# Performance work log

Hardware: AMD Instinct MI355X
Metric: run time of the kernel (lower is better)

## Reference

```python
import jax, jax.numpy as jnp
import numpy as np

E = 8        # num experts
TOPK = 2
H = 1024     # hidden size
F = 4096     # ffn hidden size
SL, BS = 2048, 2
TOKENS = SL * BS
N = TOKENS * TOPK          # flattened routing assignments
CAP = (TOPK * TOKENS) // E # expert_capacity with capacity_factor=1.0


def setup_inputs() -> dict:
    key = jax.random.key(0)
    ks = jax.random.split(key, 6)
    x = jax.random.normal(ks[0], (SL, BS, H), jnp.float32)
    scores = jax.random.uniform(ks[1], (TOKENS, E), dtype=jnp.float32)
    expert_weights = jax.random.uniform(ks[2], (TOKENS, TOPK), dtype=jnp.float32)
    top_experts = jax.random.randint(ks[3], (TOKENS, TOPK), 0, E, dtype=jnp.int32)
    w1 = jax.random.normal(ks[4], (E, H, F), jnp.float32) * 0.02
    w2 = jax.random.normal(ks[5], (E, F, H), jnp.float32) * 0.02
    bias = jnp.zeros((H,), jnp.float32)
    return {"x": x, "scores": scores, "expert_weights": expert_weights,
            "top_experts": top_experts, "w1": w1, "w2": w2, "bias": bias}


def reference(x, scores, expert_weights, top_experts, w1, w2, bias):
    # --- indices_and_bins: stable sort tokens by expert, histogram, cumsum ---
    te = top_experts.reshape(-1)          # [N] int
    ew = expert_weights.reshape(-1)       # [N]
    xf = x.reshape(-1, H)                 # [TOKENS, H]

    indices = jnp.argsort(te)             # stable sort -> permutation [N]
    bin_ids = te[indices]                 # sorted expert ids [N]
    tpe = jax.ops.segment_sum(jnp.ones_like(te), te, num_segments=E)  # tokens per expert
    bins = jnp.cumsum(tpe)                # inclusive cumsum
    starts = bins - tpe                   # start offset of each expert's bin
    pos = jnp.arange(N) - starts[bin_ids] # position within expert bin [N]
    valid = pos < CAP                     # capacity drop mask
    tok = indices // TOPK                 # source token row for each assignment

    # --- binned_gather: [E, CAP, H], zero padded, tokens beyond capacity dropped ---
    dst = jnp.where(valid, pos, CAP)      # out-of-range -> dropped via mode='drop'
    buf = jnp.zeros((E, CAP, H), x.dtype).at[bin_ids, dst].set(xf[tok], mode='drop')

    # --- grouped MLP: per-expert gelu FFN ---
    h = jax.nn.gelu(jnp.einsum('ech,ehf->ecf', buf, w1), approximate=False)
    y = jnp.einsum('ecf,efh->ech', h, w2)

    # --- binned_scatter: weighted un-permute back to token order ---
    vals = y[bin_ids, jnp.where(valid, pos, 0)]                      # [N, H]
    w = jnp.where(valid, ew[indices], 0.0)[:, None]
    out = jnp.zeros((TOKENS, H), x.dtype).at[tok].add(vals * w)

    return out.reshape(x.shape) + bias
```

## Files before the change

### kernel.cpp

```cpp
#include <hip/hip_runtime.h>
#include <hip/hip_bf16.h>
#include <math.h>

#define NE 8
#define TOPK 2
#define HD 1024
#define FD 4096
#define NTOK 4096
#define NASSIGN 8192
#define CAP 1024

typedef __attribute__((ext_vector_type(8))) short short8;
typedef __attribute__((ext_vector_type(4))) float f32x4;
typedef __attribute__((ext_vector_type(4))) unsigned short us4;
typedef __attribute__((ext_vector_type(4))) unsigned int u32x4;

__device__ __forceinline__ unsigned short f2bf(float f) {
  unsigned u = __float_as_uint(f);
  u += 0x7fffu + ((u >> 16) & 1u);
  return (unsigned short)(u >> 16);
}

__device__ __forceinline__ void load_lds16(const void* g, void* l) {
  __builtin_amdgcn_global_load_lds((const __attribute__((address_space(1))) void*)g,
                                   (__attribute__((address_space(3))) void*)l, 16, 0, 0);
}

__global__ __launch_bounds__(256)
void transpose_convert(const float* __restrict__ W, unsigned short* __restrict__ Wt,
                       int R, int C) {
  __shared__ float tile[64][65];
  int e = blockIdx.z;
  W  += (size_t)e * R * C;
  Wt += (size_t)e * R * C;
  int c0 = blockIdx.x * 64, r0 = blockIdx.y * 64;
  int tx = threadIdx.x & 15, ty = threadIdx.x >> 4;
#pragma unroll
  for (int i = 0; i < 4; ++i) {
    f32x4 v = *(const f32x4*)(W + (size_t)(r0 + ty + i * 16) * C + c0 + tx * 4);
    tile[ty + i * 16][tx * 4 + 0] = v.x;
    tile[ty + i * 16][tx * 4 + 1] = v.y;
    tile[ty + i * 16][tx * 4 + 2] = v.z;
    tile[ty + i * 16][tx * 4 + 3] = v.w;
  }
  __syncthreads();
#pragma unroll
  for (int i = 0; i < 4; ++i) {
    int c = ty + i * 16;
    us4 o;
    o.x = f2bf(tile[tx * 4 + 0][c]);
    o.y = f2bf(tile[tx * 4 + 1][c]);
    o.z = f2bf(tile[tx * 4 + 2][c]);
    o.w = f2bf(tile[tx * 4 + 3][c]);
    *(us4*)(Wt + (size_t)(c0 + c) * R + r0 + tx * 4) = o;
  }
}

__global__ __launch_bounds__(1024)
void routing_kernel(const int* __restrict__ te, int* __restrict__ rankA,
                    int* __restrict__ srcTok, int* __restrict__ counts) {
  __shared__ uint4 pref[1024];
  int t = threadIdx.x;
  int myTe[8];
  unsigned lc[4] = {0, 0, 0, 0};
#pragma unroll
  for (int j = 0; j < 8; ++j) {
    int ee = te[t * 8 + j];
    myTe[j] = ee;
    lc[ee >> 1] += 1u << ((ee & 1) * 16);
  }
  uint4 inc;
  inc.x = lc[0]; inc.y = lc[1]; inc.z = lc[2]; inc.w = lc[3];
  pref[t] = inc;
  __syncthreads();
  for (int d = 1; d < 1024; d <<= 1) {
    uint4 add;
    bool has = (t >= d);
    if (has) add = pref[t - d];
    __syncthreads();
    if (has) {
      inc.x += add.x; inc.y += add.y; inc.z += add.z; inc.w += add.w;
      pref[t] = inc;
    }
    __syncthreads();
  }
  unsigned ex[4] = {inc.x - lc[0], inc.y - lc[1], inc.z - lc[2], inc.w - lc[3]};
  uint4 tot = pref[1023];
  int run[8];
#pragma unroll
  for (int eidx = 0; eidx < 8; ++eidx)
    run[eidx] = (ex[eidx >> 1] >> ((eidx & 1) * 16)) & 0xffff;
#pragma unroll
  for (int j = 0; j < 8; ++j) {
    int ee = myTe[j];
    int r = run[ee]++;
    rankA[t * 8 + j] = r;
    if (r < CAP) srcTok[ee * CAP + r] = (t * 8 + j) >> 1;
  }
  if (t < 8) {
    unsigned tt[4] = {tot.x, tot.y, tot.z, tot.w};
    counts[t] = (tt[t >> 1] >> ((t & 1) * 16)) & 0xffff;
  }
}

__global__ __launch_bounds__(128)
void gather_kernel(const float* __restrict__ x, const int* __restrict__ srcTok,
                   const int* __restrict__ counts, unsigned short* __restrict__ buf) {
  int row = blockIdx.x;
  int e = row >> 10;
  int c = row & (CAP - 1);
  int t = threadIdx.x;
  unsigned short* dst = buf + (size_t)row * HD + t * 8;
  if (c < counts[e]) {
    const float* src = x + (size_t)srcTok[row] * HD + t * 8;
    f32x4 v0 = *(const f32x4*)src;
    f32x4 v1 = *(const f32x4*)(src + 4);
    u32x4 o;
    o.x = f2bf(v0.x) | ((unsigned)f2bf(v0.y) << 16);
    o.y = f2bf(v0.z) | ((unsigned)f2bf(v0.w) << 16);
    o.z = f2bf(v1.x) | ((unsigned)f2bf(v1.y) << 16);
    o.w = f2bf(v1.z) | ((unsigned)f2bf(v1.w) << 16);
    *(u32x4*)dst = o;
  } else {
    u32x4 z = {0, 0, 0, 0};
    *(u32x4*)dst = z;
  }
}

template <int KTOT, int NDIM, int OMODE, int KSPLIT>
__global__ __launch_bounds__(512, 2)
void gemm256(const unsigned short* __restrict__ Ab, const unsigned short* __restrict__ Bb,
             void* __restrict__ Cv) {
  constexpr int KLOC = KTOT / KSPLIT;
  constexpr int NT = KLOC / 32;
  constexpr int GX = CAP / 256;
  constexpr int GY = NDIM / 256;
  constexpr int NWG = GX * GY * NE * KSPLIT;
  __shared__ char smem[4 * 32768];

  int orig = blockIdx.x;
  int wg = (orig & 7) * (NWG / 8) + (orig >> 3);
  int bx = wg % GX;
  int by = (wg / GX) % GY;
  int zz = wg / (GX * GY);
  int ks = zz % KSPLIT;
  int e  = zz / KSPLIT;

  const unsigned short* A  = Ab + (size_t)e * CAP * KTOT;
  const unsigned short* Bt = Bb + (size_t)e * NDIM * KTOT;
  int bm = bx * 256, bn = by * 256;
  int kbase = ks * KLOC;

  int tid = threadIdx.x;
  int lane = tid & 63;
  int w = tid >> 6;
  int wr = w >> 2, wc = w & 3;
  int l15 = lane & 15, lq = lane >> 4;

  unsigned sw = (unsigned)((lq ^ ((l15 >> 1) & 3)) << 4);
  unsigned aoff[8], boff[4];
#pragma unroll
  for (int m = 0; m < 8; ++m)
    aoff[m] = (unsigned)((wr * 128 + m * 16 + l15) * 64) + sw;
#pragma unroll
  for (int n = 0; n < 4; ++n)
    boff[n] = 16384u + (unsigned)((wc * 64 + n * 16 + l15) * 64) + sw;

  const char *sA0, *sA1, *sB0, *sB1;
  unsigned dA0, dA1, dB0, dB1;
  {
    int i0 = tid, i1 = 512 + tid;
    int r0_ = i0 >> 2, r1_ = i1 >> 2;
    unsigned kb0 = ((unsigned)(i0 & 3) ^ (((unsigned)r0_ >> 1) & 3u)) << 4;
    unsigned kb1 = ((unsigned)(i1 & 3) ^ (((unsigned)r1_ >> 1) & 3u)) << 4;
    sA0 = (const char*)(A  + (size_t)(bm + r0_) * KTOT + kbase) + kb0;
    sA1 = (const char*)(A  + (size_t)(bm + r1_) * KTOT + kbase) + kb1;
    sB0 = (const char*)(Bt + (size_t)(bn + r0_) * KTOT + kbase) + kb0;
    sB1 = (const char*)(Bt + (size_t)(bn + r1_) * KTOT + kbase) + kb1;
    dA0 = (unsigned)i0 * 16;  dA1 = (unsigned)i1 * 16;
    dB0 = 16384u + (unsigned)i0 * 16; dB1 = 16384u + (unsigned)i1 * 16;
  }

#pragma unroll
  for (int tt = 0; tt < 3; ++tt) {
    char* db = smem + tt * 32768;
    load_lds16(sA0 + tt * 64, db + dA0);
    load_lds16(sA1 + tt * 64, db + dA1);
    load_lds16(sB0 + tt * 64, db + dB0);
    load_lds16(sB1 + tt * 64, db + dB1);
  }
  sA0 += 192; sA1 += 192; sB0 += 192; sB1 += 192;
  asm volatile("s_waitcnt vmcnt(8)\ns_barrier" ::: "memory");

  f32x4 acc[8][4] = {};

#pragma unroll 1
  for (int t = 0; t < NT; ++t) {
    const char* rb = smem + (t & 3) * 32768;
    short8 af[8], bf[4];
#pragma unroll
    for (int n = 0; n < 4; ++n) bf[n] = *(const short8*)(rb + boff[n]);
#pragma unroll
    for (int m = 0; m < 8; ++m) af[m] = *(const short8*)(rb + aoff[m]);
    if (t + 3 < NT) {
      char* db = smem + ((t + 3) & 3) * 32768;
      load_lds16(sA0, db + dA0);
      load_lds16(sA1, db + dA1);
      load_lds16(sB0, db + dB0);
      load_lds16(sB1, db + dB1);
      sA0 += 64; sA1 += 64; sB0 += 64; sB1 += 64;
    }
#pragma unroll
    for (int m = 0; m < 8; ++m)
#pragma unroll
      for (int n = 0; n < 4; ++n)
        acc[m][n] = __builtin_amdgcn_mfma_f32_16x16x32_bf16(af[m], bf[n], acc[m][n], 0, 0, 0);
    if (t + 3 < NT)       asm volatile("s_waitcnt vmcnt(8)" ::: "memory");
    else if (t == NT - 3) asm volatile("s_waitcnt vmcnt(4)" ::: "memory");
    else if (t == NT - 2) asm volatile("s_waitcnt vmcnt(0)" ::: "memory");
    asm volatile("s_barrier" ::: "memory");
  }

  int r0 = bm + wr * 128 + lq * 4;
  int c0 = bn + wc * 64 + l15;
  if (OMODE == 1) {
    unsigned short* C = (unsigned short*)Cv + (size_t)e * CAP * NDIM;
#pragma unroll
    for (int m = 0; m < 8; ++m)
#pragma unroll
      for (int n = 0; n < 4; ++n)
#pragma unroll
        for (int j = 0; j < 4; ++j) {
          float v = acc[m][n][j];
          float y = 0.7978845608028654f * (v + 0.044715f * v * v * v);
          float g = v / (1.0f + __expf(-2.0f * y));
          C[(size_t)(r0 + m * 16 + j) * NDIM + (c0 + n * 16)] = f2bf(g);
        }
  } else {
    unsigned short* C = (unsigned short*)Cv + ((size_t)ks * NE + e) * CAP * NDIM;
#pragma unroll
    for (int m = 0; m < 8; ++m)
#pragma unroll
      for (int n = 0; n < 4; ++n)
#pragma unroll
        for (int j = 0; j < 4; ++j)
          C[(size_t)(r0 + m * 16 + j) * NDIM + (c0 + n * 16)] = f2bf(acc[m][n][j]);
  }
}

__global__ __launch_bounds__(128)
void scatter_kernel(const unsigned short* __restrict__ y, const int* __restrict__ te,
                    const int* __restrict__ rankA, const float* __restrict__ ew,
                    const float* __restrict__ bias, float* __restrict__ out) {
  int tk = blockIdx.x;
  int t = threadIdx.x;
  f32x4 a0 = *(const f32x4*)(bias + t * 8);
  f32x4 a1 = *(const f32x4*)(bias + t * 8 + 4);
#pragma unroll
  for (int k = 0; k < TOPK; ++k) {
    int a = tk * TOPK + k;
    int r = rankA[a];
    if (r < CAP) {
      float wgt = ew[a];
      size_t rowoff = ((size_t)te[a] * CAP + r) * HD + t * 8;
      u32x4 p0 = *(const u32x4*)(y + rowoff);
      u32x4 p1 = *(const u32x4*)(y + (size_t)NE * CAP * HD + rowoff);
#pragma unroll
      for (int j = 0; j < 2; ++j) {
        unsigned u0 = p0[j], u1 = p1[j];
        a0[2 * j]     += wgt * (__uint_as_float(u0 << 16) + __uint_as_float(u1 << 16));
        a0[2 * j + 1] += wgt * (__uint_as_float(u0 & 0xffff0000u) + __uint_as_float(u1 & 0xffff0000u));
      }
#pragma unroll
      for (int j = 0; j < 2; ++j) {
        unsigned u0 = p0[2 + j], u1 = p1[2 + j];
        a1[2 * j]     += wgt * (__uint_as_float(u0 << 16) + __uint_as_float(u1 << 16));
        a1[2 * j + 1] += wgt * (__uint_as_float(u0 & 0xffff0000u) + __uint_as_float(u1 & 0xffff0000u));
      }
    }
  }
  float* o = out + (size_t)tk * HD + t * 8;
  *(f32x4*)o = a0;
  *(f32x4*)(o + 4) = a1;
}

extern "C" void kernel_launch(void* const* d_in, const int* in_sizes, int n_in,
                              void* d_out, int out_size, void* d_ws, size_t ws_size,
                              hipStream_t stream) {
  const float* x    = (const float*)d_in[0];
  const float* ew   = (const float*)d_in[2];
  const int*   te   = (const int*)d_in[3];
  const float* w1   = (const float*)d_in[4];
  const float* w2   = (const float*)d_in[5];
  const float* bias = (const float*)d_in[6];
  float* out = (float*)d_out;

  unsigned short* w1t  = (unsigned short*)d_ws;
  unsigned short* w2t  = w1t + (size_t)NE * HD * FD;
  unsigned short* bufg = w2t + (size_t)NE * HD * FD;
  unsigned short* hbuf = bufg + (size_t)NE * CAP * HD;
  unsigned short* ybuf = w1t;
  int* rankA  = (int*)(hbuf + (size_t)NE * CAP * FD);
  int* srcTok = rankA + NASSIGN;
  int* counts = srcTok + NE * CAP;

  transpose_convert<<<dim3(FD / 64, HD / 64, NE), 256, 0, stream>>>(w1, w1t, HD, FD);
  transpose_convert<<<dim3(HD / 64, FD / 64, NE), 256, 0, stream>>>(w2, w2t, FD, HD);
  routing_kernel<<<1, 1024, 0, stream>>>(te, rankA, srcTok, counts);
  gather_kernel<<<NE * CAP, 128, 0, stream>>>(x, srcTok, counts, bufg);
  gemm256<HD, FD, 1, 1><<<512, 512, 0, stream>>>(bufg, w1t, (void*)hbuf);
  gemm256<FD, HD, 2, 2><<<256, 512, 0, stream>>>(hbuf, w2t, (void*)ybuf);
  scatter_kernel<<<NTOK, 128, 0, stream>>>(ybuf, te, rankA, ew, bias, out);
}
```

Before: 268.3 us.

## Shrink GEMM tile to 256x128 with 4 waves and 3-stage LDS pipeline

Replaces the 256x256 GEMM tile (8 waves, 4 LDS buffers of 32KB, 3-deep prefetch) with a 256x128 tile run by 4 waves, using 3 LDS buffers of 24KB and 2-deep prefetch. The grid doubles to 1024 and 512 workgroups, and each workgroup uses much less LDS. The aim is better occupancy and more workgroups to balance across CUs. In exchange, each tile reuses less data, so more global and L2 traffic is needed per FLOP, and the shallower prefetch hides less latency. An unused swz helper is also added.

Measured after the change: 267.4 us. About the same (-0.3%).

```diff
diff --git a/kernel.cpp b/kernel.cpp
--- a/kernel.cpp
+++ b/kernel.cpp
@@ -24,6 +24,10 @@
 __device__ __forceinline__ void load_lds16(const void* g, void* l) {
   __builtin_amdgcn_global_load_lds((const __attribute__((address_space(1))) void*)g,
                                    (__attribute__((address_space(3))) void*)l, 16, 0, 0);
+}
+
+__device__ __forceinline__ unsigned swz(unsigned b) {
+  return b ^ (((b >> 7) & 3u) << 4);
 }
 
 __global__ __launch_bounds__(256)
@@ -128,15 +132,16 @@
 }
 
 template <int KTOT, int NDIM, int OMODE, int KSPLIT>
-__global__ __launch_bounds__(512, 2)
-void gemm256(const unsigned short* __restrict__ Ab, const unsigned short* __restrict__ Bb,
-             void* __restrict__ Cv) {
+__global__ __launch_bounds__(256, 2)
+void gemm256x128(const unsigned short* __restrict__ Ab, const unsigned short* __restrict__ Bb,
+                 void* __restrict__ Cv) {
   constexpr int KLOC = KTOT / KSPLIT;
   constexpr int NT = KLOC / 32;
   constexpr int GX = CAP / 256;
-  constexpr int GY = NDIM / 256;
+  constexpr int GY = NDIM / 128;
   constexpr int NWG = GX * GY * NE * KSPLIT;
-  __shared__ char smem[4 * 32768];
+  constexpr unsigned BUFB = 24576u;
+  __shared__ char smem[3 * 24576];
 
   int orig = blockIdx.x;
   int wg = (orig & 7) * (NWG / 8) + (orig >> 3);
@@ -148,13 +153,13 @@
 
   const unsigned short* A  = Ab + (size_t)e * CAP * KTOT;
   const unsigned short* Bt = Bb + (size_t)e * NDIM * KTOT;
-  int bm = bx * 256, bn = by * 256;
+  int bm = bx * 256, bn = by * 128;
   int kbase = ks * KLOC;
 
   int tid = threadIdx.x;
   int lane = tid & 63;
   int w = tid >> 6;
-  int wr = w >> 2, wc = w & 3;
+  int wr = w >> 1, wc = w & 1;
   int l15 = lane & 15, lq = lane >> 4;
 
   unsigned sw = (unsigned)((lq ^ ((l15 >> 1) & 3)) << 4);
@@ -166,59 +171,70 @@
   for (int n = 0; n < 4; ++n)
     boff[n] = 16384u + (unsigned)((wc * 64 + n * 16 + l15) * 64) + sw;
 
-  const char *sA0, *sA1, *sB0, *sB1;
-  unsigned dA0, dA1, dB0, dB1;
-  {
-    int i0 = tid, i1 = 512 + tid;
-    int r0_ = i0 >> 2, r1_ = i1 >> 2;
-    unsigned kb0 = ((unsigned)(i0 & 3) ^ (((unsigned)r0_ >> 1) & 3u)) << 4;
-    unsigned kb1 = ((unsigned)(i1 & 3) ^ (((unsigned)r1_ >> 1) & 3u)) << 4;
-    sA0 = (const char*)(A  + (size_t)(bm + r0_) * KTOT + kbase) + kb0;
-    sA1 = (const char*)(A  + (size_t)(bm + r1_) * KTOT + kbase) + kb1;
-    sB0 = (const char*)(Bt + (size_t)(bn + r0_) * KTOT + kbase) + kb0;
-    sB1 = (const char*)(Bt + (size_t)(bn + r1_) * KTOT + kbase) + kb1;
-    dA0 = (unsigned)i0 * 16;  dA1 = (unsigned)i1 * 16;
-    dB0 = 16384u + (unsigned)i0 * 16; dB1 = 16384u + (unsigned)i1 * 16;
-  }
-
-#pragma unroll
-  for (int tt = 0; tt < 3; ++tt) {
-    char* db = smem + tt * 32768;
-    load_lds16(sA0 + tt * 64, db + dA0);
-    load_lds16(sA1 + tt * 64, db + dA1);
-    load_lds16(sB0 + tt * 64, db + dB0);
-    load_lds16(sB1 + tt * 64, db + dB1);
-  }
-  sA0 += 192; sA1 += 192; sB0 += 192; sB1 += 192;
-  asm volatile("s_waitcnt vmcnt(8)\ns_barrier" ::: "memory");
+  const char* sA[4]; const char* sB[2];
+  unsigned dA[4], dB[2];
+#pragma unroll
+  for (int j = 0; j < 4; ++j) {
+    int idx = j * 256 + tid;
+    int r_ = idx >> 2;
+    unsigned kb = ((unsigned)(idx & 3) ^ (((unsigned)r_ >> 1) & 3u)) << 4;
+    sA[j] = (const char*)(A + (size_t)(bm + r_) * KTOT + kbase) + kb;
+    dA[j] = (unsigned)idx * 16;
+  }
+#pragma unroll
+  for (int j = 0; j < 2; ++j) {
+    int idx = j * 256 + tid;
+    int r_ = idx >> 2;
+    unsigned kb = ((unsigned)(idx & 3) ^ (((unsigned)r_ >> 1) & 3u)) << 4;
+    sB[j] = (const char*)(Bt + (size_t)(bn + r_) * KTOT + kbase) + kb;
+    dB[j] = 16384u + (unsigned)idx * 16;
+  }
+
+#pragma unroll
+  for (int tt = 0; tt < 2; ++tt) {
+    char* db = smem + tt * BUFB;
+#pragma unroll
+    for (int j = 0; j < 4; ++j) load_lds16(sA[j] + tt * 64, db + dA[j]);
+#pragma unroll
+    for (int j = 0; j < 2; ++j) load_lds16(sB[j] + tt * 64, db + dB[j]);
+  }
+#pragma unroll
+  for (int j = 0; j < 4; ++j) sA[j] += 128;
+#pragma unroll
+  for (int j = 0; j < 2; ++j) sB[j] += 128;
+  asm volatile("s_waitcnt vmcnt(6)" ::: "memory");
+  __builtin_amdgcn_s_barrier();
 
   f32x4 acc[8][4] = {};
 
+  unsigned cur = 0;
 #pragma unroll 1
   for (int t = 0; t < NT; ++t) {
-    const char* rb = smem + (t & 3) * 32768;
+    const char* rb = smem + cur;
     short8 af[8], bf[4];
 #pragma unroll
     for (int n = 0; n < 4; ++n) bf[n] = *(const short8*)(rb + boff[n]);
 #pragma unroll
     for (int m = 0; m < 8; ++m) af[m] = *(const short8*)(rb + aoff[m]);
-    if (t + 3 < NT) {
-      char* db = smem + ((t + 3) & 3) * 32768;
-      load_lds16(sA0, db + dA0);
-      load_lds16(sA1, db + dA1);
-      load_lds16(sB0, db + dB0);
-      load_lds16(sB1, db + dB1);
-      sA0 += 64; sA1 += 64; sB0 += 64; sB1 += 64;
+    if (t + 2 < NT) {
+      unsigned stg = cur + 2 * BUFB;
+      if (stg >= 3 * BUFB) stg -= 3 * BUFB;
+      char* db = smem + stg;
+#pragma unroll
+      for (int j = 0; j < 4; ++j) { load_lds16(sA[j], db + dA[j]); sA[j] += 64; }
+#pragma unroll
+      for (int j = 0; j < 2; ++j) { load_lds16(sB[j], db + dB[j]); sB[j] += 64; }
     }
 #pragma unroll
     for (int m = 0; m < 8; ++m)
 #pragma unroll
       for (int n = 0; n < 4; ++n)
         acc[m][n] = __builtin_amdgcn_mfma_f32_16x16x32_bf16(af[m], bf[n], acc[m][n], 0, 0, 0);
-    if (t + 3 < NT)       asm volatile("s_waitcnt vmcnt(8)" ::: "memory");
-    else if (t == NT - 3) asm volatile("s_waitcnt vmcnt(4)" ::: "memory");
+    if (t + 2 < NT)       asm volatile("s_waitcnt vmcnt(6)" ::: "memory");
     else if (t == NT - 2) asm volatile("s_waitcnt vmcnt(0)" ::: "memory");
     asm volatile("s_barrier" ::: "memory");
+    cur += BUFB;
+    if (cur >= 3 * BUFB) cur = 0u;
   }
 
   int r0 = bm + wr * 128 + lq * 4;
@@ -308,7 +324,7 @@
   transpose_convert<<<dim3(HD / 64, FD / 64, NE), 256, 0, stream>>>(w2, w2t, FD, HD);
   routing_kernel<<<1, 1024, 0, stream>>>(te, rankA, srcTok, counts);
   gather_kernel<<<NE * CAP, 128, 0, stream>>>(x, srcTok, counts, bufg);
-  gemm256<HD, FD, 1, 1><<<512, 512, 0, stream>>>(bufg, w1t, (void*)hbuf);
-  gemm256<FD, HD, 2, 2><<<256, 512, 0, stream>>>(hbuf, w2t, (void*)ybuf);
+  gemm256x128<HD, FD, 1, 1><<<1024, 256, 0, stream>>>(bufg, w1t, (void*)hbuf);
+  gemm256x128<FD, HD, 2, 2><<<512, 256, 0, stream>>>(hbuf, w2t, (void*)ybuf);
   scatter_kernel<<<NTOK, 128, 0, stream>>>(ybuf, te, rankA, ew, bias, out);
 }
```
